# Performance work log

Hardware: AMD Instinct MI355X
Metric: run time of the kernel (lower is better)

The kernel has to match this reference:

```python
import jax, jax.numpy as jnp
import numpy as np

N_NODES = 100000
N_EDGES = 1600000
D_IN = 128
D_OUT = 128


def setup_inputs() -> dict:
    key = jax.random.key(0)
    k1, k2, k3, k4, k5, k6 = jax.random.split(key, 6)
    x = jax.random.normal(k1, (N_NODES, D_IN), dtype=jnp.float32)
    edge_row = jax.random.randint(k2, (N_EDGES,), 0, N_NODES, dtype=jnp.int64)
    edge_col = jax.random.randint(k3, (N_EDGES,), 0, N_NODES, dtype=jnp.int64)
    edge_val = jax.random.uniform(k4, (N_EDGES,), dtype=jnp.float32)
    # Xavier-uniform init for weight, zeros for bias (matches reset_parameters)
    limit = float(np.sqrt(6.0 / (D_IN + D_OUT)))
    weight = jax.random.uniform(k5, (D_IN, D_OUT), minval=-limit, maxval=limit, dtype=jnp.float32)
    bias = jax.random.normal(k6, (D_OUT,), dtype=jnp.float32) * 0.02
    return {"x": x, "edge_row": edge_row, "edge_col": edge_col,
            "edge_val": edge_val, "weight": weight, "bias": bias}


def reference(x, edge_row, edge_col, edge_val, weight, bias):
    # dropout(p=0.0) is identity in eval -> omitted
    support = x @ weight                       # [N, D_OUT] dense GEMM
    # SpMM: out[r] = sum_{e: row[e]==r} val[e] * support[col[e]]
    messages = edge_val[:, None] * support[edge_col]   # [E, D_OUT]
    out = jax.ops.segment_sum(messages, edge_row, num_segments=N_NODES)
    return out + bias
```

## Files before the change

kernel.cpp:

```cpp
#include <hip/hip_runtime.h>


#define DMODEL 128
#define LDSTRIDE 136
#define CAP 64
#define NB_INSERT 2048

typedef __attribute__((ext_vector_type(8))) short short8_t;
typedef __attribute__((ext_vector_type(4))) float float4_t;

__device__ inline short f2bf(float f) {
    unsigned u = __float_as_uint(f);
    return (short)((u + 0x7FFFu + ((u >> 16) & 1u)) >> 16);
}

__global__ __launch_bounds__(256) void fused_gemm_insert(
    const float* __restrict__ x, const float* __restrict__ w,
    unsigned short* __restrict__ support,
    const int* __restrict__ erow, const int* __restrict__ ecol,
    const float* __restrict__ eval,
    int* __restrict__ counts, int2* __restrict__ edata,
    int n_nodes, int n_edges, int nb_g)
{
    __shared__ short wt_lds[DMODEL * LDSTRIDE];

    if (blockIdx.x >= nb_g) {
        int t = (blockIdx.x - nb_g) * 256 + threadIdx.x;
        for (int e = t; e < n_edges; e += NB_INSERT * 256) {
            int r = erow[e];
            int rk = atomicAdd(&counts[r], 1);
            if (rk < CAP) {
                int2 d; d.x = ecol[e]; d.y = __float_as_int(eval[e]);
                edata[(size_t)r * CAP + rk] = d;
            }
        }
        return;
    }

    {
        const float4* w4 = (const float4*)w;
        #pragma unroll
        for (int i = 0; i < 16; ++i) {
            int idx4 = threadIdx.x + i * 256;
            int k = idx4 >> 5;
            int n = (idx4 & 31) * 4;
            float4 v = w4[idx4];
            wt_lds[(n + 0) * LDSTRIDE + k] = f2bf(v.x);
            wt_lds[(n + 1) * LDSTRIDE + k] = f2bf(v.y);
            wt_lds[(n + 2) * LDSTRIDE + k] = f2bf(v.z);
            wt_lds[(n + 3) * LDSTRIDE + k] = f2bf(v.w);
        }
    }
    __syncthreads();

    int row0 = blockIdx.x * 64;
    int wv   = threadIdx.x >> 6;
    int lane = threadIdx.x & 63;
    int m    = lane & 15;
    int g    = lane >> 4;

    int rowA = row0 + wv * 16 + m;
    int rowAc = rowA < n_nodes ? rowA : n_nodes - 1;
    const float* xr = x + (size_t)rowAc * DMODEL + g * 8;
    short8_t af[4];
    #pragma unroll
    for (int kc = 0; kc < 4; ++kc) {
        float4 u0 = *(const float4*)(xr + kc * 32);
        float4 u1 = *(const float4*)(xr + kc * 32 + 4);
        short8_t a;
        a[0] = f2bf(u0.x); a[1] = f2bf(u0.y); a[2] = f2bf(u0.z); a[3] = f2bf(u0.w);
        a[4] = f2bf(u1.x); a[5] = f2bf(u1.y); a[6] = f2bf(u1.z); a[7] = f2bf(u1.w);
        af[kc] = a;
    }

    float4_t acc[8];
    #pragma unroll
    for (int nt = 0; nt < 8; ++nt) {
        float4_t z = {0.f, 0.f, 0.f, 0.f};
        acc[nt] = z;
        int n = nt * 16 + m;
        #pragma unroll
        for (int kc = 0; kc < 4; ++kc) {
            short8_t bf = *(const short8_t*)&wt_lds[n * LDSTRIDE + kc * 32 + g * 8];
            acc[nt] = __builtin_amdgcn_mfma_f32_16x16x32_bf16(af[kc], bf, acc[nt], 0, 0, 0);
        }
    }

    int orow = row0 + wv * 16 + g * 4;
    #pragma unroll
    for (int r = 0; r < 4; ++r) {
        int row = orow + r;
        if (row < n_nodes) {
            #pragma unroll
            for (int nt = 0; nt < 8; ++nt)
                support[(size_t)row * DMODEL + nt * 16 + m] = (unsigned short)f2bf(acc[nt][r]);
        }
    }
}

__global__ __launch_bounds__(256) void aggregate_kernel(
    const int* __restrict__ counts, const int2* __restrict__ edata,
    const uint4* __restrict__ sup, const float* __restrict__ bias,
    float* __restrict__ out, int n_nodes)
{
    int node = (blockIdx.x * blockDim.x + threadIdx.x) >> 6;
    if (node >= n_nodes) return;
    int lane = threadIdx.x & 63;
    int sub  = lane >> 4;
    int q    = lane & 15;

    int len = counts[node];
    if (len > CAP) len = CAP;
    const int2* ed = edata + (size_t)node * CAP;

    float acc[8];
    #pragma unroll
    for (int k = 0; k < 8; ++k) acc[k] = 0.f;

    #define EDGE_FMA(d, p)                                                   \
        {                                                                    \
            float v = __int_as_float((d).y);                                 \
            acc[0] = fmaf(v, __uint_as_float((p).x << 16), acc[0]);          \
            acc[1] = fmaf(v, __uint_as_float((p).x & 0xFFFF0000u), acc[1]);  \
            acc[2] = fmaf(v, __uint_as_float((p).y << 16), acc[2]);          \
            acc[3] = fmaf(v, __uint_as_float((p).y & 0xFFFF0000u), acc[3]);  \
            acc[4] = fmaf(v, __uint_as_float((p).z << 16), acc[4]);          \
            acc[5] = fmaf(v, __uint_as_float((p).z & 0xFFFF0000u), acc[5]);  \
            acc[6] = fmaf(v, __uint_as_float((p).w << 16), acc[6]);          \
            acc[7] = fmaf(v, __uint_as_float((p).w & 0xFFFF0000u), acc[7]);  \
        }

    int i = sub;
    for (; i + 4 < len; i += 8) {
        int2 d0 = ed[i];
        int2 d1 = ed[i + 4];
        uint4 p0 = sup[(size_t)d0.x * 16 + q];
        uint4 p1 = sup[(size_t)d1.x * 16 + q];
        EDGE_FMA(d0, p0);
        EDGE_FMA(d1, p1);
    }
    if (i < len) {
        int2 d0 = ed[i];
        uint4 p0 = sup[(size_t)d0.x * 16 + q];
        EDGE_FMA(d0, p0);
    }
    #undef EDGE_FMA

    #pragma unroll
    for (int k = 0; k < 8; ++k) {
        acc[k] += __shfl_xor(acc[k], 16);
        acc[k] += __shfl_xor(acc[k], 32);
    }

    if (sub == 0) {
        float4 b0 = ((const float4*)bias)[q * 2];
        float4 b1 = ((const float4*)bias)[q * 2 + 1];
        float4 o0 = make_float4(acc[0] + b0.x, acc[1] + b0.y, acc[2] + b0.z, acc[3] + b0.w);
        float4 o1 = make_float4(acc[4] + b1.x, acc[5] + b1.y, acc[6] + b1.z, acc[7] + b1.w);
        ((float4*)out)[(size_t)node * 32 + q * 2]     = o0;
        ((float4*)out)[(size_t)node * 32 + q * 2 + 1] = o1;
    }
}

extern "C" void kernel_launch(void* const* d_in, const int* in_sizes, int n_in,
                              void* d_out, int out_size, void* d_ws, size_t ws_size,
                              hipStream_t stream) {
    const float* x      = (const float*)d_in[0];
    const int*   erow   = (const int*)d_in[1];
    const int*   ecol   = (const int*)d_in[2];
    const float* eval   = (const float*)d_in[3];
    const float* weight = (const float*)d_in[4];
    const float* bias   = (const float*)d_in[5];
    float* out = (float*)d_out;

    const int n_nodes = in_sizes[0] / DMODEL;
    const int n_edges = in_sizes[3];

    char* ws = (char*)d_ws;
    unsigned short* support = (unsigned short*)ws;  ws += (size_t)n_nodes * DMODEL * 2;
    int*  counts = (int*)ws;                        ws += ((size_t)n_nodes * 4 + 15) & ~15ull;
    int2* edata  = (int2*)ws;                       ws += (size_t)n_nodes * CAP * 8;

    const int nb_g = (n_nodes + 63) / 64;

    hipMemsetAsync(counts, 0, (size_t)n_nodes * sizeof(int), stream);
    fused_gemm_insert<<<nb_g + NB_INSERT, 256, 0, stream>>>(
        x, weight, support, erow, ecol, eval, counts, edata, n_nodes, n_edges, nb_g);
    aggregate_kernel<<<(n_nodes + 3) / 4, 256, 0, stream>>>(
        counts, edata, (const uint4*)support, bias, out, n_nodes);
}
```

Measured before the change: 266.0 us.

## Split fused GEMM/insert kernel and pre-swizzle weights into MFMA fragment layout

After: 307.2 us. +15.5%, slower.

```diff
diff --git a/kernel.cpp b/kernel.cpp
--- a/kernel.cpp
+++ b/kernel.cpp
@@ -2,9 +2,7 @@
 
 
 #define DMODEL 128
-#define LDSTRIDE 136
 #define CAP 64
-#define NB_INSERT 2048
 
 typedef __attribute__((ext_vector_type(8))) short short8_t;
 typedef __attribute__((ext_vector_type(4))) float float4_t;
@@ -14,54 +12,54 @@
     return (short)((u + 0x7FFFu + ((u >> 16) & 1u)) >> 16);
 }
 
-__global__ __launch_bounds__(256) void fused_gemm_insert(
-    const float* __restrict__ x, const float* __restrict__ w,
-    unsigned short* __restrict__ support,
-    const int* __restrict__ erow, const int* __restrict__ ecol,
-    const float* __restrict__ eval,
-    int* __restrict__ counts, int2* __restrict__ edata,
-    int n_nodes, int n_edges, int nb_g)
-{
-    __shared__ short wt_lds[DMODEL * LDSTRIDE];
+__global__ __launch_bounds__(256) void prep_w(const float* __restrict__ w,
+                                              unsigned short* __restrict__ wsw) {
+    int t = threadIdx.x;
+    #pragma unroll
+    for (int i = 0; i < 8; ++i) {
+        int c = t + i * 256;
+        int lane = c & 63;
+        int kcnt = c >> 6;
+        int kc = kcnt & 3, nt = kcnt >> 2;
+        int n  = nt * 16 + (lane & 15);
+        int k0 = kc * 32 + (lane >> 4) * 8;
+        short8_t v;
+        #pragma unroll
+        for (int j = 0; j < 8; ++j)
+            v[j] = f2bf(w[(size_t)(k0 + j) * DMODEL + n]);
+        *(short8_t*)&wsw[(size_t)c * 8] = v;
+    }
+}
 
-    if (blockIdx.x >= nb_g) {
-        int t = (blockIdx.x - nb_g) * 256 + threadIdx.x;
-        for (int e = t; e < n_edges; e += NB_INSERT * 256) {
-            int r = erow[e];
-            int rk = atomicAdd(&counts[r], 1);
-            if (rk < CAP) {
-                int2 d; d.x = ecol[e]; d.y = __float_as_int(eval[e]);
-                edata[(size_t)r * CAP + rk] = d;
-            }
-        }
-        return;
+__global__ __launch_bounds__(256) void insert_kernel(const int* __restrict__ erow,
+                                                     const int* __restrict__ ecol,
+                                                     const float* __restrict__ eval,
+                                                     int* __restrict__ counts,
+                                                     int2* __restrict__ edata,
+                                                     int n_edges) {
+    int e = blockIdx.x * blockDim.x + threadIdx.x;
+    if (e >= n_edges) return;
+    int r = erow[e];
+    int rk = atomicAdd(&counts[r], 1);
+    if (rk < CAP) {
+        int2 d; d.x = ecol[e]; d.y = __float_as_int(eval[e]);
+        edata[(size_t)r * CAP + rk] = d;
     }
+}
 
-    {
-        const float4* w4 = (const float4*)w;
-        #pragma unroll
-        for (int i = 0; i < 16; ++i) {
-            int idx4 = threadIdx.x + i * 256;
-            int k = idx4 >> 5;
-            int n = (idx4 & 31) * 4;
-            float4 v = w4[idx4];
-            wt_lds[(n + 0) * LDSTRIDE + k] = f2bf(v.x);
-            wt_lds[(n + 1) * LDSTRIDE + k] = f2bf(v.y);
-            wt_lds[(n + 2) * LDSTRIDE + k] = f2bf(v.z);
-            wt_lds[(n + 3) * LDSTRIDE + k] = f2bf(v.w);
-        }
-    }
-    __syncthreads();
-
-    int row0 = blockIdx.x * 64;
+__global__ __launch_bounds__(256) void gemm_kernel(const float* __restrict__ x,
+                                                   const unsigned short* __restrict__ wsw,
+                                                   unsigned short* __restrict__ support,
+                                                   int n_nodes) {
     int wv   = threadIdx.x >> 6;
     int lane = threadIdx.x & 63;
     int m    = lane & 15;
     int g    = lane >> 4;
 
-    int rowA = row0 + wv * 16 + m;
+    int rowA  = blockIdx.x * 64 + wv * 16 + m;
     int rowAc = rowA < n_nodes ? rowA : n_nodes - 1;
     const float* xr = x + (size_t)rowAc * DMODEL + g * 8;
+
     short8_t af[4];
     #pragma unroll
     for (int kc = 0; kc < 4; ++kc) {
@@ -73,20 +71,21 @@
         af[kc] = a;
     }
 
+    const short8_t* wf = (const short8_t*)wsw;
+
     float4_t acc[8];
     #pragma unroll
     for (int nt = 0; nt < 8; ++nt) {
         float4_t z = {0.f, 0.f, 0.f, 0.f};
         acc[nt] = z;
-        int n = nt * 16 + m;
         #pragma unroll
         for (int kc = 0; kc < 4; ++kc) {
-            short8_t bf = *(const short8_t*)&wt_lds[n * LDSTRIDE + kc * 32 + g * 8];
+            short8_t bf = wf[(nt * 4 + kc) * 64 + lane];
             acc[nt] = __builtin_amdgcn_mfma_f32_16x16x32_bf16(af[kc], bf, acc[nt], 0, 0, 0);
         }
     }
 
-    int orow = row0 + wv * 16 + g * 4;
+    int orow = blockIdx.x * 64 + wv * 16 + g * 4;
     #pragma unroll
     for (int r = 0; r < 4; ++r) {
         int row = orow + r;
@@ -178,14 +177,14 @@
 
     char* ws = (char*)d_ws;
     unsigned short* support = (unsigned short*)ws;  ws += (size_t)n_nodes * DMODEL * 2;
+    unsigned short* wsw     = (unsigned short*)ws;  ws += (size_t)DMODEL * DMODEL * 2;
     int*  counts = (int*)ws;                        ws += ((size_t)n_nodes * 4 + 15) & ~15ull;
     int2* edata  = (int2*)ws;                       ws += (size_t)n_nodes * CAP * 8;
 
-    const int nb_g = (n_nodes + 63) / 64;
-
     hipMemsetAsync(counts, 0, (size_t)n_nodes * sizeof(int), stream);
-    fused_gemm_insert<<<nb_g + NB_INSERT, 256, 0, stream>>>(
-        x, weight, support, erow, ecol, eval, counts, edata, n_nodes, n_edges, nb_g);
+    prep_w<<<1, 256, 0, stream>>>(weight, wsw);
+    insert_kernel<<<(n_edges + 255) / 256, 256, 0, stream>>>(erow, ecol, eval, counts, edata, n_edges);
+    gemm_kernel<<<(n_nodes + 63) / 64, 256, 0, stream>>>(x, wsw, support, n_nodes);
     aggregate_kernel<<<(n_nodes + 3) / 4, 256, 0, stream>>>(
         counts, edata, (const uint4*)support, bias, out, n_nodes);
 }
```
